# Optimization experiments

Hardware: AMD Instinct MI355X
Metric: run time of the kernel (lower is better)

## Reference

```python
import jax, jax.numpy as jnp
import numpy as np

S, T, H, D = 4096, 4096, 16, 64
N_EMBD = H * D

def setup_inputs() -> dict:
    key = jax.random.key(0)
    kq, kk, kv, kw = jax.random.split(key, 4)
    q = jax.random.normal(kq, (S, H, D), dtype=jnp.float32)
    k = jax.random.normal(kk, (T, H, D), dtype=jnp.float32)
    v = jax.random.normal(kv, (T, H, D), dtype=jnp.float32)
    # GPT-2 style init: std = 0.02 / sqrt(2 * n_layer), n_layer = 24
    W_proj = jax.random.normal(kw, (N_EMBD, N_EMBD), dtype=jnp.float32) * (0.02 / np.sqrt(2 * 24))
    return {"q": q, "k": k, "v": v, "W_proj": W_proj}

def reference(q, k, v, W_proj):
    s, h, d = q.shape
    t = k.shape[0]
    # causal bias: mask positions where query index < key index (future keys)
    causal_bias = (jnp.arange(s)[:, None] < jnp.arange(t)[None, :]).astype(jnp.float32) * -10000.0
    scale = 1.0 / jnp.sqrt(jnp.float32(d))
    # [h, s, t] scores in fp32 (matches original .astype(jnp.float32))
    scores = jnp.einsum('shd,thd->hst', q, k).astype(jnp.float32) * scale + causal_bias
    attn = jax.nn.softmax(scores, axis=-1).astype(q.dtype)
    # dropout p=0 / inference -> identity
    out = jnp.einsum('hst,thd->shd', attn, v).reshape(s, h * d)
    # nn.Linear (no bias) vmapped over tokens: y = x @ W.T
    return out @ W_proj.T
```

## Files before the change

kernel.cpp:

```cpp
#include <hip/hip_runtime.h>

#define S_LEN 4096
#define NH 16
#define DH 64
#define NE 1024

typedef __bf16 bf16_t;
typedef __bf16 bf16x8 __attribute__((ext_vector_type(8)));
typedef __bf16 bf16x4 __attribute__((ext_vector_type(4)));
typedef __bf16 bf16x2 __attribute__((ext_vector_type(2)));
typedef float  f32x4  __attribute__((ext_vector_type(4)));

#define QSCALE 0.180336879f

__global__ __launch_bounds__(256) void pack_all(const float* __restrict__ q,
                                                const float* __restrict__ k,
                                                const float* __restrict__ w,
                                                const float* __restrict__ v,
                                                bf16_t* __restrict__ qb,
                                                bf16_t* __restrict__ kb,
                                                bf16_t* __restrict__ wb,
                                                bf16_t* __restrict__ vt) {
    __shared__ bf16_t tile[64][65];
    const int bid = blockIdx.x;
    if (bid < 4096) {
        const int tid = bid * 256 + threadIdx.x;
        const int e = tid * 4;
        const int s = e >> 10;
        const int c = e & (NE - 1);
        const int h = c >> 6;
        const int d = c & (DH - 1);
        const int o = (h * S_LEN + s) * DH + d;
        float4 qv = *(const float4*)(q + e);
        float4 kv = *(const float4*)(k + e);
        bf16x4 qo, ko;
        qo[0] = (bf16_t)(qv.x * QSCALE); qo[1] = (bf16_t)(qv.y * QSCALE);
        qo[2] = (bf16_t)(qv.z * QSCALE); qo[3] = (bf16_t)(qv.w * QSCALE);
        ko[0] = (bf16_t)kv.x; ko[1] = (bf16_t)kv.y; ko[2] = (bf16_t)kv.z; ko[3] = (bf16_t)kv.w;
        *(bf16x4*)(qb + o) = qo;
        *(bf16x4*)(kb + o) = ko;
        if (tid < (NE * NE / 4)) {
            float4 wv = *(const float4*)(w + tid * 4);
            bf16x4 wo;
            wo[0] = (bf16_t)wv.x; wo[1] = (bf16_t)wv.y; wo[2] = (bf16_t)wv.z; wo[3] = (bf16_t)wv.w;
            *(bf16x4*)(wb + tid * 4) = wo;
        }
    } else {
        const int vb = bid - 4096;
        const int h  = vb >> 6;
        const int t0 = (vb & 63) * 64;
        const int r  = threadIdx.x >> 6;
        const int cl = threadIdx.x & 63;
#pragma unroll
        for (int rep = 0; rep < 16; ++rep) {
            int i = rep * 4 + r;
            tile[cl][i] = (bf16_t)v[(t0 + i) * NE + h * DH + cl];
        }
        __syncthreads();
        const int r2  = threadIdx.x >> 5;
        const int cl2 = (threadIdx.x & 31) * 2;
        const int ip = (cl2 & 32) + ((cl2 >> 2) & 1) * 16 + ((cl2 >> 4) & 1) * 8 +
                       ((cl2 >> 3) & 1) * 4 + (cl2 & 3);
#pragma unroll
        for (int rep = 0; rep < 8; ++rep) {
            int d = rep * 8 + r2;
            bf16x2 out;
            out[0] = tile[d][ip];
            out[1] = tile[d][ip + 1];
            *(bf16x2*)(vt + (h * DH + d) * S_LEN + t0 + cl2) = out;
        }
    }
}

__global__ __launch_bounds__(256, 4) void attn(const bf16_t* __restrict__ qb,
                                               const bf16_t* __restrict__ kb,
                                               const bf16_t* __restrict__ vt,
                                               float* __restrict__ po,
                                               float* __restrict__ ls) {
    __shared__ __align__(16) bf16_t kbuf[2][64 * 72];
    __shared__ __align__(16) bf16_t vbuf[2][64 * 72];

    const int tid  = threadIdx.x;
    const int wave = tid >> 6;
    const int lane = tid & 63;
    const int l15  = lane & 15;
    const int quad = lane >> 4;
    const int h = blockIdx.x;
    const int x = blockIdx.y;

    const int sA = x;
    const int sB = 31 - x;
    const int n0 = x + 1;
    const int b1 = sB + 1;
    const int N  = 33;

    const bf16_t* __restrict__ qh = qb + h * (S_LEN * DH);
    const bf16_t* __restrict__ kh = kb + h * (S_LEN * DH);
    const bf16_t* __restrict__ vh = vt + h * (DH * S_LEN);

    const int row0 = tid >> 3;
    const int tc8  = (tid & 7) * 8;
    const int stg  = row0 * 72 + tc8;
    const int frg  = l15 * 72 + quad * 8;

    f32x4 o_acc[2][4];
    f32x4 rs[2];
    bf16x8 qA[2][2];
    bf16x8 ones;
#pragma unroll
    for (int e = 0; e < 8; ++e) ones[e] = (bf16_t)1.0f;
    int s0 = sA * 128 + wave * 32;

    auto load_q = [&](int s0_) {
#pragma unroll
        for (int g = 0; g < 2; ++g)
#pragma unroll
            for (int dc = 0; dc < 2; ++dc)
                qA[g][dc] = *(const bf16x8*)(qh + (s0_ + g * 16 + l15) * DH + dc * 32 + quad * 8);
    };
    auto reset_acc = [&]() {
#pragma unroll
        for (int g = 0; g < 2; ++g) {
#pragma unroll
            for (int db = 0; db < 4; ++db) o_acc[g][db] = (f32x4){0.f, 0.f, 0.f, 0.f};
            rs[g] = (f32x4){0.f, 0.f, 0.f, 0.f};
        }
    };
    auto epilogue = [&](int s0_, int slot) {
        float* poz = po + (size_t)(slot * NH + h) * S_LEN * DH;
#pragma unroll
        for (int g = 0; g < 2; ++g)
#pragma unroll
            for (int db = 0; db < 4; ++db)
#pragma unroll
                for (int r = 0; r < 4; ++r)
                    poz[(s0_ + g * 16 + quad * 4 + r) * DH + db * 16 + l15] = o_acc[g][db][r];
        if (l15 == 0) {
            float* lsz = ls + (size_t)(slot * NH + h) * S_LEN;
#pragma unroll
            for (int g = 0; g < 2; ++g)
#pragma unroll
                for (int r = 0; r < 4; ++r) lsz[s0_ + g * 16 + quad * 4 + r] = rs[g][r];
        }
    };

    load_q(s0);
    reset_acc();

    {
        bf16x8 kr0 = *(const bf16x8*)(kh + row0 * DH + tc8);
        bf16x8 kr1 = *(const bf16x8*)(kh + (row0 + 32) * DH + tc8);
        bf16x8 vr0 = *(const bf16x8*)(vh + row0 * S_LEN + tc8);
        bf16x8 vr1 = *(const bf16x8*)(vh + (row0 + 32) * S_LEN + tc8);
        *(bf16x8*)(kbuf[0] + stg) = kr0;
        *(bf16x8*)(kbuf[0] + stg + 32 * 72) = kr1;
        *(bf16x8*)(vbuf[0] + stg) = vr0;
        *(bf16x8*)(vbuf[0] + stg + 32 * 72) = vr1;
    }
    __syncthreads();

#pragma unroll 2
    for (int j = 0; j < N; ++j) {
        if (j == n0) {
            epilogue(s0, 0);
            s0 = sB * 128 + wave * 32;
            load_q(s0);
            reset_acc();
        }
        const int t0 = (j < n0 ? j : b1 + (j - n0)) * 64;
        const bf16_t* kb_ = kbuf[j & 1];
        const bf16_t* vb_ = vbuf[j & 1];

        const bool pf = (j + 1 < N);
        int tn = 0;
        bf16x8 kr0n, kr1n, vr0n, vr1n;
        if (pf) {
            const int jn = j + 1;
            tn = (jn < n0 ? jn : b1 + (jn - n0)) * 64;
            kr0n = *(const bf16x8*)(kh + (tn + row0) * DH + tc8);
            kr1n = *(const bf16x8*)(kh + (tn + row0 + 32) * DH + tc8);
        }

        if (t0 <= s0 + 31) {
            const bool edge = (t0 + 63 > s0);
            bf16x8 pA[2][2];

#pragma unroll
            for (int kc = 0; kc < 2; ++kc) {
                const int chA = kc * 2;
                bf16x8 kB00 = *(const bf16x8*)(kb_ + frg + (chA + 0) * (16 * 72));
                bf16x8 kB01 = *(const bf16x8*)(kb_ + frg + (chA + 0) * (16 * 72) + 32);
                bf16x8 kB10 = *(const bf16x8*)(kb_ + frg + (chA + 1) * (16 * 72));
                bf16x8 kB11 = *(const bf16x8*)(kb_ + frg + (chA + 1) * (16 * 72) + 32);
                f32x4 cA[2], cB[2];
#pragma unroll
                for (int g = 0; g < 2; ++g) {
                    f32x4 z = (f32x4){0.f, 0.f, 0.f, 0.f};
                    z = __builtin_amdgcn_mfma_f32_16x16x32_bf16(kB00, qA[g][0], z, 0, 0, 0);
                    z = __builtin_amdgcn_mfma_f32_16x16x32_bf16(kB01, qA[g][1], z, 0, 0, 0);
                    cA[g] = z;
                    z = (f32x4){0.f, 0.f, 0.f, 0.f};
                    z = __builtin_amdgcn_mfma_f32_16x16x32_bf16(kB10, qA[g][0], z, 0, 0, 0);
                    z = __builtin_amdgcn_mfma_f32_16x16x32_bf16(kB11, qA[g][1], z, 0, 0, 0);
                    cB[g] = z;
                }
#pragma unroll
                for (int g = 0; g < 2; ++g) {
                    const int query = s0 + g * 16 + l15;
#pragma unroll
                    for (int r = 0; r < 4; ++r) {
                        float a = cA[g][r];
                        float b = cB[g][r];
                        if (edge) {
                            const int keyA = t0 + chA * 16 + quad * 4 + r;
                            if (keyA > query)      a = -INFINITY;
                            if (keyA + 16 > query) b = -INFINITY;
                        }
                        pA[g][kc][r]     = (bf16_t)exp2f(a);
                        pA[g][kc][4 + r] = (bf16_t)exp2f(b);
                    }
                }
            }

#pragma unroll
            for (int g = 0; g < 2; ++g) {
                rs[g] = __builtin_amdgcn_mfma_f32_16x16x32_bf16(pA[g][0], ones, rs[g], 0, 0, 0);
                rs[g] = __builtin_amdgcn_mfma_f32_16x16x32_bf16(pA[g][1], ones, rs[g], 0, 0, 0);
            }

            if (pf) {
                vr0n = *(const bf16x8*)(vh + row0 * S_LEN + tn + tc8);
                vr1n = *(const bf16x8*)(vh + (row0 + 32) * S_LEN + tn + tc8);
            }

#pragma unroll
            for (int db = 0; db < 4; ++db) {
                bf16x8 vB0 = *(const bf16x8*)(vb_ + frg + db * (16 * 72));
                bf16x8 vB1 = *(const bf16x8*)(vb_ + frg + db * (16 * 72) + 32);
#pragma unroll
                for (int g = 0; g < 2; ++g) {
                    o_acc[g][db] = __builtin_amdgcn_mfma_f32_16x16x32_bf16(pA[g][0], vB0, o_acc[g][db], 0, 0, 0);
                    o_acc[g][db] = __builtin_amdgcn_mfma_f32_16x16x32_bf16(pA[g][1], vB1, o_acc[g][db], 0, 0, 0);
                }
            }
        } else if (pf) {
            vr0n = *(const bf16x8*)(vh + row0 * S_LEN + tn + tc8);
            vr1n = *(const bf16x8*)(vh + (row0 + 32) * S_LEN + tn + tc8);
        }

        if (pf) {
            bf16_t* kd = kbuf[(j + 1) & 1];
            bf16_t* vd = vbuf[(j + 1) & 1];
            *(bf16x8*)(kd + stg) = kr0n;
            *(bf16x8*)(kd + stg + 32 * 72) = kr1n;
            *(bf16x8*)(vd + stg) = vr0n;
            *(bf16x8*)(vd + stg + 32 * 72) = vr1n;
        }
        __syncthreads();
    }

    epilogue(s0, 1);
}

__global__ __launch_bounds__(256) void combine(const float* __restrict__ po,
                                               const float* __restrict__ ls,
                                               bf16_t* __restrict__ xb) {
    const int idx = blockIdx.x * 256 + threadIdx.x;
    const int row = idx >> 8;
    const int c   = (idx & 255) * 4;
    const int h   = c >> 6;
    const int d   = c & 63;
    const size_t base0 = (size_t)(h) * S_LEN * DH + row * DH + d;
    const size_t base1 = (size_t)(NH + h) * S_LEN * DH + row * DH + d;
    float4 o0 = *(const float4*)(po + base0);
    float4 o1 = *(const float4*)(po + base1);
    float l = ls[(size_t)h * S_LEN + row] + ls[(size_t)(NH + h) * S_LEN + row];
    float inv = 1.0f / l;
    bf16x4 out;
    out[0] = (bf16_t)((o0.x + o1.x) * inv);
    out[1] = (bf16_t)((o0.y + o1.y) * inv);
    out[2] = (bf16_t)((o0.z + o1.z) * inv);
    out[3] = (bf16_t)((o0.w + o1.w) * inv);
    *(bf16x4*)(xb + (size_t)row * NE + c) = out;
}

__global__ __launch_bounds__(256, 4) void proj(const bf16_t* __restrict__ xb,
                                               const bf16_t* __restrict__ wb,
                                               float* __restrict__ y) {
    __shared__ __align__(16) bf16_t wbuf[2][64 * 72];
    const int tid  = threadIdx.x;
    const int wave = tid >> 6;
    const int lane = tid & 63;
    const int l15  = lane & 15;
    const int quad = lane >> 4;
    const int m0 = blockIdx.x * 128 + wave * 32;
    const int n0 = blockIdx.y * 64;

    const int row0 = tid >> 3;
    const int tc8  = (tid & 7) * 8;

    f32x4 acc[2][4];
#pragma unroll
    for (int g = 0; g < 2; ++g)
#pragma unroll
        for (int nb = 0; nb < 4; ++nb) acc[g][nb] = (f32x4){0.f, 0.f, 0.f, 0.f};

    {
        bf16x8 wr0 = *(const bf16x8*)(wb + (n0 + row0) * NE + tc8);
        bf16x8 wr1 = *(const bf16x8*)(wb + (n0 + row0 + 32) * NE + tc8);
        *(bf16x8*)(wbuf[0] + row0 * 72 + tc8) = wr0;
        *(bf16x8*)(wbuf[0] + (row0 + 32) * 72 + tc8) = wr1;
    }
    bf16x8 a[2][2];
#pragma unroll
    for (int g = 0; g < 2; ++g)
#pragma unroll
        for (int kc = 0; kc < 2; ++kc)
            a[g][kc] = *(const bf16x8*)(xb + (m0 + g * 16 + l15) * NE + kc * 32 + quad * 8);
    __syncthreads();

    for (int kt = 0; kt < 16; ++kt) {
        const bf16_t* wb_ = wbuf[kt & 1];
        const bool pf = (kt + 1 < 16);
        bf16x8 wr0, wr1, an[2][2];
        if (pf) {
            const int kn = (kt + 1) * 64;
            wr0 = *(const bf16x8*)(wb + (n0 + row0) * NE + kn + tc8);
            wr1 = *(const bf16x8*)(wb + (n0 + row0 + 32) * NE + kn + tc8);
#pragma unroll
            for (int g = 0; g < 2; ++g)
#pragma unroll
                for (int kc = 0; kc < 2; ++kc)
                    an[g][kc] = *(const bf16x8*)(xb + (m0 + g * 16 + l15) * NE + kn + kc * 32 + quad * 8);
        }

#pragma unroll
        for (int nb = 0; nb < 4; ++nb)
#pragma unroll
            for (int kc = 0; kc < 2; ++kc) {
                bf16x8 b = *(const bf16x8*)(wb_ + (nb * 16 + l15) * 72 + kc * 32 + quad * 8);
#pragma unroll
                for (int g = 0; g < 2; ++g)
                    acc[g][nb] = __builtin_amdgcn_mfma_f32_16x16x32_bf16(a[g][kc], b, acc[g][nb], 0, 0, 0);
            }

        if (pf) {
            *(bf16x8*)(wbuf[(kt + 1) & 1] + row0 * 72 + tc8) = wr0;
            *(bf16x8*)(wbuf[(kt + 1) & 1] + (row0 + 32) * 72 + tc8) = wr1;
#pragma unroll
            for (int g = 0; g < 2; ++g)
#pragma unroll
                for (int kc = 0; kc < 2; ++kc) a[g][kc] = an[g][kc];
        }
        __syncthreads();
    }

#pragma unroll
    for (int g = 0; g < 2; ++g)
#pragma unroll
        for (int nb = 0; nb < 4; ++nb)
#pragma unroll
            for (int r = 0; r < 4; ++r)
                y[(m0 + g * 16 + quad * 4 + r) * NE + n0 + nb * 16 + l15] = acc[g][nb][r];
}

extern "C" void kernel_launch(void* const* d_in, const int* in_sizes, int n_in,
                              void* d_out, int out_size, void* d_ws, size_t ws_size,
                              hipStream_t stream) {
    const float* q = (const float*)d_in[0];
    const float* k = (const float*)d_in[1];
    const float* v = (const float*)d_in[2];
    const float* w = (const float*)d_in[3];
    float* y = (float*)d_out;

    bf16_t* ws = (bf16_t*)d_ws;
    bf16_t* qb = ws;
    bf16_t* kb = qb + 4 * 1024 * 1024;
    bf16_t* vt = kb + 4 * 1024 * 1024;
    bf16_t* wb = vt + 4 * 1024 * 1024;
    bf16_t* xb = wb + 1024 * 1024;
    float*  po = (float*)(xb + 4 * 1024 * 1024);
    float*  ls = po + (size_t)2 * NH * S_LEN * DH;

    pack_all<<<dim3(4096 + 1024), dim3(256), 0, stream>>>(q, k, w, v, qb, kb, wb, vt);
    attn<<<dim3(NH, 32), dim3(256), 0, stream>>>(qb, kb, vt, po, ls);
    combine<<<dim3(4096), dim3(256), 0, stream>>>(po, ls, xb);
    proj<<<dim3(S_LEN / 128, NE / 64), dim3(256), 0, stream>>>(xb, wb, y);
}
```

Baseline: 198.5 us.

## Split paired query tiles of attention into separate blocks via grid z

Each attention block previously processed two causal query tiles sequentially (a short and a long one) and wrote both partial outputs. The kernel now launches a third grid dimension so each block handles only one of the two tiles, doubling the number of blocks. This is meant to raise occupancy and GPU fill, since the previous grid covered only about half of the available block slots. It gives up the built-in load balancing of pairing tiles and adds per-block setup overhead.

```diff
diff --git a/kernel.cpp b/kernel.cpp
--- a/kernel.cpp
+++ b/kernel.cpp
@@ -87,6 +87,7 @@
     const int quad = lane >> 4;
     const int h = blockIdx.x;
     const int x = blockIdx.y;
+    const int z = blockIdx.z;
 
     const int sA = x;
     const int sB = 31 - x;
@@ -94,6 +95,10 @@
     const int b1 = sB + 1;
     const int N  = 33;
 
+    const int jb = z ? n0 : 0;
+    const int je = z ? N  : n0;
+    const int s0 = (z ? sB : sA) * 128 + wave * 32;
+
     const bf16_t* __restrict__ qh = qb + h * (S_LEN * DH);
     const bf16_t* __restrict__ kh = kb + h * (S_LEN * DH);
     const bf16_t* __restrict__ vh = vt + h * (DH * S_LEN);
@@ -109,74 +114,45 @@
     bf16x8 ones;
 #pragma unroll
     for (int e = 0; e < 8; ++e) ones[e] = (bf16_t)1.0f;
-    int s0 = sA * 128 + wave * 32;
-
-    auto load_q = [&](int s0_) {
-#pragma unroll
-        for (int g = 0; g < 2; ++g)
-#pragma unroll
-            for (int dc = 0; dc < 2; ++dc)
-                qA[g][dc] = *(const bf16x8*)(qh + (s0_ + g * 16 + l15) * DH + dc * 32 + quad * 8);
-    };
-    auto reset_acc = [&]() {
-#pragma unroll
-        for (int g = 0; g < 2; ++g) {
-#pragma unroll
-            for (int db = 0; db < 4; ++db) o_acc[g][db] = (f32x4){0.f, 0.f, 0.f, 0.f};
-            rs[g] = (f32x4){0.f, 0.f, 0.f, 0.f};
-        }
-    };
-    auto epilogue = [&](int s0_, int slot) {
-        float* poz = po + (size_t)(slot * NH + h) * S_LEN * DH;
-#pragma unroll
-        for (int g = 0; g < 2; ++g)
-#pragma unroll
-            for (int db = 0; db < 4; ++db)
-#pragma unroll
-                for (int r = 0; r < 4; ++r)
-                    poz[(s0_ + g * 16 + quad * 4 + r) * DH + db * 16 + l15] = o_acc[g][db][r];
-        if (l15 == 0) {
-            float* lsz = ls + (size_t)(slot * NH + h) * S_LEN;
-#pragma unroll
-            for (int g = 0; g < 2; ++g)
-#pragma unroll
-                for (int r = 0; r < 4; ++r) lsz[s0_ + g * 16 + quad * 4 + r] = rs[g][r];
-        }
-    };
-
-    load_q(s0);
-    reset_acc();
+
+    auto t0_of = [&](int j) { return (j < n0 ? j : b1 + (j - n0)) * 64; };
+
+#pragma unroll
+    for (int g = 0; g < 2; ++g)
+#pragma unroll
+        for (int dc = 0; dc < 2; ++dc)
+            qA[g][dc] = *(const bf16x8*)(qh + (s0 + g * 16 + l15) * DH + dc * 32 + quad * 8);
+#pragma unroll
+    for (int g = 0; g < 2; ++g) {
+#pragma unroll
+        for (int db = 0; db < 4; ++db) o_acc[g][db] = (f32x4){0.f, 0.f, 0.f, 0.f};
+        rs[g] = (f32x4){0.f, 0.f, 0.f, 0.f};
+    }
 
     {
-        bf16x8 kr0 = *(const bf16x8*)(kh + row0 * DH + tc8);
-        bf16x8 kr1 = *(const bf16x8*)(kh + (row0 + 32) * DH + tc8);
-        bf16x8 vr0 = *(const bf16x8*)(vh + row0 * S_LEN + tc8);
-        bf16x8 vr1 = *(const bf16x8*)(vh + (row0 + 32) * S_LEN + tc8);
-        *(bf16x8*)(kbuf[0] + stg) = kr0;
-        *(bf16x8*)(kbuf[0] + stg + 32 * 72) = kr1;
-        *(bf16x8*)(vbuf[0] + stg) = vr0;
-        *(bf16x8*)(vbuf[0] + stg + 32 * 72) = vr1;
+        const int t0 = t0_of(jb);
+        bf16x8 kr0 = *(const bf16x8*)(kh + (t0 + row0) * DH + tc8);
+        bf16x8 kr1 = *(const bf16x8*)(kh + (t0 + row0 + 32) * DH + tc8);
+        bf16x8 vr0 = *(const bf16x8*)(vh + row0 * S_LEN + t0 + tc8);
+        bf16x8 vr1 = *(const bf16x8*)(vh + (row0 + 32) * S_LEN + t0 + tc8);
+        *(bf16x8*)(kbuf[jb & 1] + stg) = kr0;
+        *(bf16x8*)(kbuf[jb & 1] + stg + 32 * 72) = kr1;
+        *(bf16x8*)(vbuf[jb & 1] + stg) = vr0;
+        *(bf16x8*)(vbuf[jb & 1] + stg + 32 * 72) = vr1;
     }
     __syncthreads();
 
 #pragma unroll 2
-    for (int j = 0; j < N; ++j) {
-        if (j == n0) {
-            epilogue(s0, 0);
-            s0 = sB * 128 + wave * 32;
-            load_q(s0);
-            reset_acc();
-        }
-        const int t0 = (j < n0 ? j : b1 + (j - n0)) * 64;
+    for (int j = jb; j < je; ++j) {
+        const int t0 = t0_of(j);
         const bf16_t* kb_ = kbuf[j & 1];
         const bf16_t* vb_ = vbuf[j & 1];
 
-        const bool pf = (j + 1 < N);
+        const bool pf = (j + 1 < je);
         int tn = 0;
         bf16x8 kr0n, kr1n, vr0n, vr1n;
         if (pf) {
-            const int jn = j + 1;
-            tn = (jn < n0 ? jn : b1 + (jn - n0)) * 64;
+            tn = t0_of(j + 1);
             kr0n = *(const bf16x8*)(kh + (tn + row0) * DH + tc8);
             kr1n = *(const bf16x8*)(kh + (tn + row0 + 32) * DH + tc8);
         }
@@ -195,14 +171,14 @@
                 f32x4 cA[2], cB[2];
 #pragma unroll
                 for (int g = 0; g < 2; ++g) {
-                    f32x4 z = (f32x4){0.f, 0.f, 0.f, 0.f};
-                    z = __builtin_amdgcn_mfma_f32_16x16x32_bf16(kB00, qA[g][0], z, 0, 0, 0);
-                    z = __builtin_amdgcn_mfma_f32_16x16x32_bf16(kB01, qA[g][1], z, 0, 0, 0);
-                    cA[g] = z;
-                    z = (f32x4){0.f, 0.f, 0.f, 0.f};
-                    z = __builtin_amdgcn_mfma_f32_16x16x32_bf16(kB10, qA[g][0], z, 0, 0, 0);
-                    z = __builtin_amdgcn_mfma_f32_16x16x32_bf16(kB11, qA[g][1], z, 0, 0, 0);
-                    cB[g] = z;
+                    f32x4 zv = (f32x4){0.f, 0.f, 0.f, 0.f};
+                    zv = __builtin_amdgcn_mfma_f32_16x16x32_bf16(kB00, qA[g][0], zv, 0, 0, 0);
+                    zv = __builtin_amdgcn_mfma_f32_16x16x32_bf16(kB01, qA[g][1], zv, 0, 0, 0);
+                    cA[g] = zv;
+                    zv = (f32x4){0.f, 0.f, 0.f, 0.f};
+                    zv = __builtin_amdgcn_mfma_f32_16x16x32_bf16(kB10, qA[g][0], zv, 0, 0, 0);
+                    zv = __builtin_amdgcn_mfma_f32_16x16x32_bf16(kB11, qA[g][1], zv, 0, 0, 0);
+                    cB[g] = zv;
                 }
 #pragma unroll
                 for (int g = 0; g < 2; ++g) {
@@ -259,7 +235,23 @@
         __syncthreads();
     }
 
-    epilogue(s0, 1);
+    {
+        float* poz = po + (size_t)(z * NH + h) * S_LEN * DH;
+#pragma unroll
+        for (int g = 0; g < 2; ++g)
+#pragma unroll
+            for (int r = 0; r < 4; ++r)
+#pragma unroll
+                for (int db = 0; db < 4; ++db)
+                    poz[(s0 + g * 16 + quad * 4 + r) * DH + db * 16 + l15] = o_acc[g][db][r];
+        if (l15 == 0) {
+            float* lsz = ls + (size_t)(z * NH + h) * S_LEN;
+#pragma unroll
+            for (int g = 0; g < 2; ++g)
+#pragma unroll
+                for (int r = 0; r < 4; ++r) lsz[s0 + g * 16 + quad * 4 + r] = rs[g][r];
+        }
+    }
 }
 
 __global__ __launch_bounds__(256) void combine(const float* __restrict__ po,
@@ -383,7 +375,7 @@
     float*  ls = po + (size_t)2 * NH * S_LEN * DH;
 
     pack_all<<<dim3(4096 + 1024), dim3(256), 0, stream>>>(q, k, w, v, qb, kb, wb, vt);
-    attn<<<dim3(NH, 32), dim3(256), 0, stream>>>(qb, kb, vt, po, ls);
+    attn<<<dim3(NH, 32, 2), dim3(256), 0, stream>>>(qb, kb, vt, po, ls);
     combine<<<dim3(4096), dim3(256), 0, stream>>>(po, ls, xb);
     proj<<<dim3(S_LEN / 128, NE / 64), dim3(256), 0, stream>>>(xb, wb, y);
 }
```

Result: slower. 229.6 us (+15.7%).
